# Performance work log

Hardware: AMD Instinct MI355X
Metric: run time of the kernel (lower is better)

The kernel has to match this reference:

```python
import jax, jax.numpy as jnp
import numpy as np

N, E, D, G = 100000, 600000, 128, 256  # nodes, edges, feat dim, num graphs
EPS = 1e-5


def graph_norm(x, batch, weight, bias, mean_scale):
    # PyG GraphNorm: per-graph mean/var with learnable mean_scale
    counts = jax.ops.segment_sum(jnp.ones((x.shape[0],), x.dtype), batch, num_segments=G)
    counts = jnp.maximum(counts, 1.0)[:, None]  # [G,1]
    mean = jax.ops.segment_sum(x, batch, num_segments=G) / counts  # [G,D]
    out = x - mean[batch] * mean_scale  # [N,D]
    var = jax.ops.segment_sum(out * out, batch, num_segments=G) / counts  # [G,D]
    inv_std = jax.lax.rsqrt(var + EPS)[batch]  # [N,D]
    return weight * out * inv_std + bias


def sage_conv_max(x, edge_index, w_l, b_l, w_r):
    # SAGEConv(aggr='max'): gather x[src], scatter-max into dst, then two linears
    src, dst = edge_index[0], edge_index[1]
    agg = jax.ops.segment_max(x[src], dst, num_segments=N)  # [N,D], -inf for empty
    agg = jnp.where(jnp.isfinite(agg), agg, 0.0)  # PyG fills empty segments with 0
    return agg @ w_l.T + b_l + x @ w_r.T


def setup_inputs() -> dict:
    key = jax.random.key(0)
    ks = jax.random.split(key, 6)
    x = jax.random.normal(ks[0], (N, D), dtype=jnp.float32)
    edge_index = jax.random.randint(ks[1], (2, E), 0, N, dtype=jnp.int64)
    batch = jnp.sort(jax.random.randint(ks[2], (N,), 0, G, dtype=jnp.int64))
    s = 1.0 / np.sqrt(D)
    return {
        "x": x,
        "edge_index": edge_index,
        "batch": batch,
        "n1_w": jnp.ones((D,), jnp.float32),
        "n1_b": jnp.zeros((D,), jnp.float32),
        "n1_ms": jnp.ones((D,), jnp.float32),
        "n2_w": jnp.ones((D,), jnp.float32),
        "n2_b": jnp.zeros((D,), jnp.float32),
        "n2_ms": jnp.ones((D,), jnp.float32),
        "w_l": jax.random.uniform(ks[3], (D, D), jnp.float32, -s, s),
        "b_l": jax.random.uniform(ks[4], (D,), jnp.float32, -s, s),
        "w_r": jax.random.uniform(ks[5], (D, D), jnp.float32, -s, s),
    }


def reference(x, edge_index, batch, n1_w, n1_b, n1_ms, n2_w, n2_b, n2_ms, w_l, b_l, w_r):
    h = graph_norm(x, batch, n1_w, n1_b, n1_ms)
    h = sage_conv_max(h, edge_index, w_l, b_l, w_r)
    h = jax.nn.relu(x + h)
    h = graph_norm(h, batch, n2_w, n2_b, n2_ms)
    return h
```

## Files before the change

### kernel.cpp

```cpp
#include <hip/hip_runtime.h>
#include <math.h>

#define NN 100000
#define EE 600000
#define DD 128
#define GG 256
#define EPSV 1e-5f

typedef __attribute__((ext_vector_type(8))) __bf16 bf16x8;
typedef __attribute__((ext_vector_type(16))) float f32x16;
typedef __attribute__((ext_vector_type(4))) unsigned short us4;

#define OFF_A1      0
#define OFF_B1      131072
#define OFF_A2      262144
#define OFF_B2      393216
#define OFF_DEG     524288
#define OFF_ROWPTR  924288
#define OFF_CURSOR  1324352
#define OFF_BSUMS   1724352
#define OFF_CNT     1726400
#define OFF_ELIST   1728448
#define OFF_WB      4128448
#define OFF_H1B     4193984
#define WS_NEED_A   (OFF_H1B + 25600000ULL)

#define NB_STATS 782
#define NB_EDGE  2344
#define NB_H1B   12500
#define NB1024   98
#define NT32     3125

__device__ __forceinline__ int lower_bound_i(const int* __restrict__ a, int n, int v) {
    int lo = 0, hi = n;
    while (lo < hi) { int mid = (lo + hi) >> 1; if (a[mid] < v) lo = mid + 1; else hi = mid; }
    return lo;
}

__device__ __forceinline__ unsigned short f2bf(float f) {
    unsigned int u = __float_as_uint(f);
    unsigned int r = u + 0x7fffu + ((u >> 16) & 1u);
    return (unsigned short)(r >> 16);
}

__device__ __forceinline__ void stats_body(
    const float* __restrict__ X, const int* __restrict__ batch,
    float* __restrict__ Sg, float* __restrict__ Qg, int blk)
{
    int t = threadIdx.x;
    int rl = t >> 5, fq = t & 31;
    int r0 = blk * 128;
    int rend = r0 + 128; if (rend > NN) rend = NN;
    __shared__ float ls[8 * 128];
    __shared__ float lq[8 * 128];
    int g0 = batch[r0], g1 = batch[rend - 1];
    const float4* X4 = (const float4*)X;
    for (int g = g0; g <= g1; ++g) {
        int sa = (g == g0) ? r0   : lower_bound_i(batch, NN, g);
        int sb = (g == g1) ? rend : lower_bound_i(batch, NN, g + 1);
        float s0 = 0.f, s1 = 0.f, s2 = 0.f, s3 = 0.f;
        float q0 = 0.f, q1 = 0.f, q2 = 0.f, q3 = 0.f;
        for (int r = sa + rl; r < sb; r += 8) {
            float4 v = X4[r * 32 + fq];
            s0 += v.x; s1 += v.y; s2 += v.z; s3 += v.w;
            q0 += v.x * v.x; q1 += v.y * v.y; q2 += v.z * v.z; q3 += v.w * v.w;
        }
        ls[rl * 128 + fq * 4 + 0] = s0; ls[rl * 128 + fq * 4 + 1] = s1;
        ls[rl * 128 + fq * 4 + 2] = s2; ls[rl * 128 + fq * 4 + 3] = s3;
        lq[rl * 128 + fq * 4 + 0] = q0; lq[rl * 128 + fq * 4 + 1] = q1;
        lq[rl * 128 + fq * 4 + 2] = q2; lq[rl * 128 + fq * 4 + 3] = q3;
        __syncthreads();
        if (t < 32) {
            #pragma unroll
            for (int k = 0; k < 4; k++) {
                float as = 0.f, aq = 0.f;
                #pragma unroll
                for (int j = 0; j < 8; j++) { as += ls[j * 128 + t * 4 + k]; aq += lq[j * 128 + t * 4 + k]; }
                atomicAdd(&Sg[g * DD + t * 4 + k], as);
                atomicAdd(&Qg[g * DD + t * 4 + k], aq);
            }
        }
        __syncthreads();
    }
}

__global__ __launch_bounds__(256) void stats_p1(
    const float* __restrict__ X, const int* __restrict__ batch,
    float* __restrict__ Sg, float* __restrict__ Qg)
{
    stats_body(X, batch, Sg, Qg, blockIdx.x);
}

__global__ __launch_bounds__(256) void statsdeg_kernel(
    const float* __restrict__ X, const int* __restrict__ batch,
    float* __restrict__ Sg, float* __restrict__ Qg,
    const int* __restrict__ dst, int* __restrict__ deg)
{
    int b = blockIdx.x;
    if (b < NB_STATS) { stats_body(X, batch, Sg, Qg, b); return; }
    int e = (b - NB_STATS) * 256 + threadIdx.x;
    if (e < EE) atomicAdd(&deg[dst[e]], 1);
}

__global__ __launch_bounds__(128) void finalize_kernel(
    const int* __restrict__ batch, float* S, float* Q,
    const float* __restrict__ w, const float* __restrict__ bb, const float* __restrict__ ms,
    unsigned short* __restrict__ wb, const float* __restrict__ wl, const float* __restrict__ wr,
    int* __restrict__ cnt, int doW)
{
    int g = blockIdx.x;
    if (g >= GG) {
        if (!doW) return;
        const float* W = (g == GG) ? wl : wr;
        int kofs = (g == GG) ? 0 : 128;
        for (int tt = threadIdx.x; tt < DD * 32; tt += 128) {
            int j = tt >> 5, k4 = tt & 31;
            float4 v = ((const float4*)W)[j * 32 + k4];
            us4 o = { f2bf(v.x), f2bf(v.y), f2bf(v.z), f2bf(v.w) };
            *(us4*)&wb[j * 256 + kofs + k4 * 4] = o;
        }
        return;
    }
    __shared__ int sh[2];
    if (threadIdx.x == 0) { sh[0] = lower_bound_i(batch, NN, g); sh[1] = lower_bound_i(batch, NN, g + 1); }
    __syncthreads();
    int c_n = sh[1] - sh[0];
    if (cnt && threadIdx.x == 0) cnt[g] = c_n;
    float c = (float)(c_n > 0 ? c_n : 1);
    float inv_c = 1.0f / c;
    int d = threadIdx.x;
    float m  = S[g * DD + d] * inv_c;
    float qm = Q[g * DD + d] * inv_c;
    float sc = ms[d];
    float var = qm - m * m * sc * (2.0f - sc);
    float Ad = w[d] * rsqrtf(var + EPSV);
    S[g * DD + d] = Ad;
    Q[g * DD + d] = bb[d] - Ad * m * sc;
}

__global__ __launch_bounds__(256) void h1bscan_kernel(
    const float* __restrict__ X, const int* __restrict__ batch,
    const float* __restrict__ A1, const float* __restrict__ B1, unsigned short* __restrict__ h1b,
    const int* __restrict__ deg, int* __restrict__ bsums)
{
    int blk = blockIdx.x;
    if (blk < NB_H1B) {
        int f = blk * 256 + threadIdx.x;
        int i = f >> 5, c = f & 31;
        int g = batch[i];
        float4 v = ((const float4*)X)[f];
        float4 a = ((const float4*)A1)[g * 32 + c];
        float4 b = ((const float4*)B1)[g * 32 + c];
        us4 o = { f2bf(fmaf(a.x, v.x, b.x)), f2bf(fmaf(a.y, v.y, b.y)),
                  f2bf(fmaf(a.z, v.z, b.z)), f2bf(fmaf(a.w, v.w, b.w)) };
        *(us4*)&h1b[i * DD + c * 4] = o;
        return;
    }
    int b = blk - NB_H1B, t = threadIdx.x;
    int base = b * 1024 + t * 4;
    int v = 0;
    #pragma unroll
    for (int k = 0; k < 4; k++) { int i = base + k; if (i < NN) v += deg[i]; }
    __shared__ int sd[256];
    sd[t] = v; __syncthreads();
    for (int off = 128; off > 0; off >>= 1) { if (t < off) sd[t] += sd[t + off]; __syncthreads(); }
    if (t == 0) bsums[b] = sd[0];
}

__global__ __launch_bounds__(256) void scan1(const int* __restrict__ deg, int* __restrict__ bsums) {
    int b = blockIdx.x, t = threadIdx.x;
    int base = b * 1024 + t * 4;
    int v = 0;
    #pragma unroll
    for (int k = 0; k < 4; k++) { int i = base + k; if (i < NN) v += deg[i]; }
    __shared__ int sd[256];
    sd[t] = v; __syncthreads();
    for (int off = 128; off > 0; off >>= 1) { if (t < off) sd[t] += sd[t + off]; __syncthreads(); }
    if (t == 0) bsums[b] = sd[0];
}

__global__ __launch_bounds__(256) void scan3(const int* __restrict__ deg, const int* __restrict__ bsums,
                                             int* __restrict__ rowptr, int* __restrict__ cursor) {
    int b = blockIdx.x, t = threadIdx.x;
    int boff = 0;
    for (int j = 0; j < b; j++) boff += bsums[j];
    int base = b * 1024 + t * 4;
    int d0 = 0, d1 = 0, d2 = 0, d3 = 0;
    if (base     < NN) d0 = deg[base];
    if (base + 1 < NN) d1 = deg[base + 1];
    if (base + 2 < NN) d2 = deg[base + 2];
    if (base + 3 < NN) d3 = deg[base + 3];
    int tsum = d0 + d1 + d2 + d3;
    __shared__ int sd[256];
    sd[t] = tsum; __syncthreads();
    for (int off = 1; off < 256; off <<= 1) {
        int a = (t >= off) ? sd[t - off] : 0;
        __syncthreads();
        sd[t] += a;
        __syncthreads();
    }
    int exc = sd[t] - tsum + boff;
    int p0 = exc, p1 = exc + d0, p2 = exc + d0 + d1, p3 = exc + d0 + d1 + d2;
    if (base     < NN) { rowptr[base]     = p0; cursor[base]     = p0; }
    if (base + 1 < NN) { rowptr[base + 1] = p1; cursor[base + 1] = p1; }
    if (base + 2 < NN) { rowptr[base + 2] = p2; cursor[base + 2] = p2; }
    if (base + 3 < NN) { rowptr[base + 3] = p3; cursor[base + 3] = p3; }
    if (b == 0 && t == 0) rowptr[NN] = EE;
}

__global__ __launch_bounds__(256) void fill_kernel(const int* __restrict__ src, const int* __restrict__ dst,
                                                   int* __restrict__ cursor, int* __restrict__ elist) {
    int e = blockIdx.x * 256 + threadIdx.x;
    if (e < EE) {
        int p = atomicAdd(&cursor[dst[e]], 1);
        elist[p] = src[e];
    }
}

#define USTR 264
__global__ __launch_bounds__(256) void gemm_mega(
    const float* __restrict__ X, const unsigned short* __restrict__ h1b,
    const int* __restrict__ batch, const int* __restrict__ rowptr, const int* __restrict__ elist,
    const unsigned short* __restrict__ wb, const float* __restrict__ blv,
    float* __restrict__ Sg2, float* __restrict__ Qg2, float* __restrict__ out)
{
    __shared__ unsigned short sU[32 * USTR];
    __shared__ int sBatch[32];
    int tid = threadIdx.x;
    int i0 = blockIdx.x * 32;
    int lane = tid & 63, wave = tid >> 6;
    int m = lane & 31, hf = lane >> 5;

    for (int t = tid; t < 32 * 16; t += 256) {
        int r = t >> 4, c = t & 15;
        int i = i0 + r; if (i >= NN) i = NN - 1;
        uint4 v = ((const uint4*)(h1b + (size_t)i * DD))[c];
        *(uint4*)&sU[r * USTR + 128 + c * 8] = v;
    }
    if (tid < 32) {
        int i = i0 + tid;
        sBatch[tid] = (i < NN) ? batch[i] : -1;
    }

    int hw = tid >> 5, j = tid & 31;
    for (int rr = hw; rr < 32; rr += 8) {
        int i = i0 + rr;
        int beg = 0, end = 0;
        if (i < NN) { beg = rowptr[i]; end = rowptr[i + 1]; }
        float a0 = -INFINITY, a1 = -INFINITY, a2 = -INFINITY, a3 = -INFINITY;
        int last = end - 1;
        for (int e = beg; e < end; e += 8) {
            int n[8];
            #pragma unroll
            for (int k = 0; k < 8; k++) { int t2 = e + k; n[k] = elist[t2 < last ? t2 : last]; }
            us4 p[8];
            #pragma unroll
            for (int k = 0; k < 8; k++) p[k] = *(const us4*)(h1b + (size_t)n[k] * DD + j * 4);
            #pragma unroll
            for (int k = 0; k < 8; k++) {
                a0 = fmaxf(a0, __uint_as_float((unsigned)p[k][0] << 16));
                a1 = fmaxf(a1, __uint_as_float((unsigned)p[k][1] << 16));
                a2 = fmaxf(a2, __uint_as_float((unsigned)p[k][2] << 16));
                a3 = fmaxf(a3, __uint_as_float((unsigned)p[k][3] << 16));
            }
        }
        us4 r4 = { 0, 0, 0, 0 };
        if (end > beg) {
            r4[0] = (unsigned short)(__float_as_uint(a0) >> 16);
            r4[1] = (unsigned short)(__float_as_uint(a1) >> 16);
            r4[2] = (unsigned short)(__float_as_uint(a2) >> 16);
            r4[3] = (unsigned short)(__float_as_uint(a3) >> 16);
        }
        *(us4*)&sU[rr * USTR + j * 4] = r4;
    }
    __syncthreads();

    int col = wave * 32 + m;
    const unsigned short* bcol = wb + col * 256 + hf * 8;
    const unsigned short* arow = &sU[m * USTR + hf * 8];

    f32x16 acc;
    #pragma unroll
    for (int r = 0; r < 16; r++) acc[r] = 0.f;
    #pragma unroll
    for (int s = 0; s < 16; s++) {
        bf16x8 b = *(const bf16x8*)(bcol + s * 16);
        bf16x8 a = *(const bf16x8*)(arow + s * 16);
        acc = __builtin_amdgcn_mfma_f32_32x32x16_bf16(a, b, acc, 0, 0, 0);
    }

    float blc = blv[col];
    float s_run = 0.f, q_run = 0.f;
    int cur_g = -1;
    #pragma unroll
    for (int reg = 0; reg < 16; reg++) {
        int rl = (reg & 3) + 8 * (reg >> 2) + 4 * hf;
        int i = i0 + rl;
        if (i < NN) {
            float v = X[i * DD + col] + blc + acc[reg];
            v = v > 0.f ? v : 0.f;
            out[i * DD + col] = v;
            int g = sBatch[rl];
            if (g != cur_g) {
                if (cur_g >= 0) {
                    atomicAdd(&Sg2[cur_g * DD + col], s_run);
                    atomicAdd(&Qg2[cur_g * DD + col], q_run);
                }
                cur_g = g; s_run = 0.f; q_run = 0.f;
            }
            s_run += v; q_run += v * v;
        }
    }
    if (cur_g >= 0) {
        atomicAdd(&Sg2[cur_g * DD + col], s_run);
        atomicAdd(&Qg2[cur_g * DD + col], q_run);
    }
}

__global__ __launch_bounds__(256) void apply_a(
    float* __restrict__ H, const int* __restrict__ batch,
    const float* __restrict__ Sg2, const float* __restrict__ Qg2, const int* __restrict__ cnt,
    const float* __restrict__ w2, const float* __restrict__ b2, const float* __restrict__ ms2)
{
    int f = blockIdx.x * 256 + threadIdx.x;
    if (f >= NN * 32) return;
    int i = f >> 5, c = f & 31;
    int g = batch[i];
    int cg = cnt[g];
    float invc = 1.0f / (float)(cg > 0 ? cg : 1);
    float4 S  = ((const float4*)Sg2)[g * 32 + c];
    float4 Q  = ((const float4*)Qg2)[g * 32 + c];
    float4 W  = ((const float4*)w2)[c];
    float4 Bv = ((const float4*)b2)[c];
    float4 Ms = ((const float4*)ms2)[c];
    float4 v = ((float4*)H)[f];
    {
        float mm = S.x * invc, qm = Q.x * invc;
        float A = W.x * rsqrtf(qm - mm * mm * Ms.x * (2.0f - Ms.x) + EPSV);
        v.x = fmaf(A, v.x, Bv.x - A * mm * Ms.x);
    }
    {
        float mm = S.y * invc, qm = Q.y * invc;
        float A = W.y * rsqrtf(qm - mm * mm * Ms.y * (2.0f - Ms.y) + EPSV);
        v.y = fmaf(A, v.y, Bv.y - A * mm * Ms.y);
    }
    {
        float mm = S.z * invc, qm = Q.z * invc;
        float A = W.z * rsqrtf(qm - mm * mm * Ms.z * (2.0f - Ms.z) + EPSV);
        v.z = fmaf(A, v.z, Bv.z - A * mm * Ms.z);
    }
    {
        float mm = S.w * invc, qm = Q.w * invc;
        float A = W.w * rsqrtf(qm - mm * mm * Ms.w * (2.0f - Ms.w) + EPSV);
        v.w = fmaf(A, v.w, Bv.w - A * mm * Ms.w);
    }
    ((float4*)H)[f] = v;
}

__global__ __launch_bounds__(256) void apply_b(float* __restrict__ H, const int* __restrict__ batch,
                                               const float* __restrict__ A2, const float* __restrict__ B2) {
    int f = blockIdx.x * 256 + threadIdx.x;
    if (f >= NN * 32) return;
    int i = f >> 5, c = f & 31;
    int g = batch[i];
    float4 v = ((float4*)H)[f];
    float4 a = ((const float4*)A2)[g * 32 + c];
    float4 b = ((const float4*)B2)[g * 32 + c];
    v.x = fmaf(a.x, v.x, b.x); v.y = fmaf(a.y, v.y, b.y);
    v.z = fmaf(a.z, v.z, b.z); v.w = fmaf(a.w, v.w, b.w);
    ((float4*)H)[f] = v;
}

__global__ __launch_bounds__(256) void agg_b(
    const float* __restrict__ X, const int* __restrict__ batch,
    const float* __restrict__ A1, const float* __restrict__ B1,
    const int* __restrict__ rowptr, const int* __restrict__ elist, float* __restrict__ H)
{
    int i = blockIdx.x * 2 + (threadIdx.x >> 7);
    int d = threadIdx.x & 127;
    int beg = rowptr[i], end = rowptr[i + 1];
    float acc = -INFINITY;
    int e = beg;
    for (; e + 2 <= end; e += 2) {
        int s0 = elist[e], s1 = elist[e + 1];
        int g0 = batch[s0], g1 = batch[s1];
        float v0 = fmaf(A1[g0 * DD + d], X[s0 * DD + d], B1[g0 * DD + d]);
        float v1 = fmaf(A1[g1 * DD + d], X[s1 * DD + d], B1[g1 * DD + d]);
        acc = fmaxf(acc, fmaxf(v0, v1));
    }
    for (; e < end; e++) {
        int s = elist[e]; int g = batch[s];
        acc = fmaxf(acc, fmaf(A1[g * DD + d], X[s * DD + d], B1[g * DD + d]));
    }
    if (end == beg) acc = 0.f;
    H[i * DD + d] = acc;
}

#define BM 128
#define LDT 72
__global__ __launch_bounds__(256) void gemm_b(
    const float* __restrict__ X, const int* __restrict__ batch,
    const float* __restrict__ A1, const float* __restrict__ B1,
    const float* __restrict__ wl, const float* __restrict__ blv, const float* __restrict__ wr,
    float* __restrict__ H)
{
    __shared__ unsigned short Ut[BM * LDT];
    __shared__ unsigned short Wt[DD * LDT];
    int i0 = blockIdx.x * BM;
    int tid = threadIdx.x;
    int lane = tid & 63, wave = tid >> 6;
    int wrow = (wave >> 1) * 64, wcol = (wave & 1) * 64;
    int m = lane & 31, hf = lane >> 5;

    f32x16 acc00, acc01, acc10, acc11;
    #pragma unroll
    for (int r = 0; r < 16; r++) { acc00[r] = 0.f; acc01[r] = 0.f; acc10[r] = 0.f; acc11[r] = 0.f; }

    for (int c = 0; c < 4; c++) {
        __syncthreads();
        for (int t = tid; t < BM * 16; t += 256) {
            int r = t >> 4, c4 = t & 15;
            int i = i0 + r; if (i >= NN) i = NN - 1;
            float4 v;
            if (c < 2) {
                v = ((const float4*)H)[i * 32 + c * 16 + c4];
            } else {
                int g = batch[i];
                float4 xv = ((const float4*)X)[i * 32 + (c - 2) * 16 + c4];
                float4 a = ((const float4*)A1)[g * 32 + (c - 2) * 16 + c4];
                float4 b = ((const float4*)B1)[g * 32 + (c - 2) * 16 + c4];
                v.x = fmaf(a.x, xv.x, b.x); v.y = fmaf(a.y, xv.y, b.y);
                v.z = fmaf(a.z, xv.z, b.z); v.w = fmaf(a.w, xv.w, b.w);
            }
            us4 o = { f2bf(v.x), f2bf(v.y), f2bf(v.z), f2bf(v.w) };
            *(us4*)&Ut[r * LDT + c4 * 4] = o;
        }
        {
            const float* Wsrc = (c < 2) ? wl : wr;
            int kb = (c & 1) * 16;
            for (int t = tid; t < DD * 16; t += 256) {
                int j = t >> 4, c4 = t & 15;
                float4 v = ((const float4*)Wsrc)[j * 32 + kb + c4];
                us4 o = { f2bf(v.x), f2bf(v.y), f2bf(v.z), f2bf(v.w) };
                *(us4*)&Wt[j * LDT + c4 * 4] = o;
            }
        }
        __syncthreads();
        #pragma unroll
        for (int kk = 0; kk < 4; kk++) {
            int kb2 = kk * 16 + hf * 8;
            bf16x8 a0 = *(const bf16x8*)&Ut[(wrow      + m) * LDT + kb2];
            bf16x8 a1 = *(const bf16x8*)&Ut[(wrow + 32 + m) * LDT + kb2];
            bf16x8 b0 = *(const bf16x8*)&Wt[(wcol      + m) * LDT + kb2];
            bf16x8 b1 = *(const bf16x8*)&Wt[(wcol + 32 + m) * LDT + kb2];
            acc00 = __builtin_amdgcn_mfma_f32_32x32x16_bf16(a0, b0, acc00, 0, 0, 0);
            acc01 = __builtin_amdgcn_mfma_f32_32x32x16_bf16(a0, b1, acc01, 0, 0, 0);
            acc10 = __builtin_amdgcn_mfma_f32_32x32x16_bf16(a1, b0, acc10, 0, 0, 0);
            acc11 = __builtin_amdgcn_mfma_f32_32x32x16_bf16(a1, b1, acc11, 0, 0, 0);
        }
    }

    int col0 = wcol + m, col1 = wcol + 32 + m;
    float bl0 = blv[col0], bl1 = blv[col1];
    #pragma unroll
    for (int reg = 0; reg < 16; reg++) {
        int rl = (reg & 3) + 8 * (reg >> 2) + 4 * hf;
        int ia = i0 + wrow + rl;
        int ib = i0 + wrow + 32 + rl;
        if (ia < NN) {
            float v0 = X[ia * DD + col0] + bl0 + acc00[reg];
            float v1 = X[ia * DD + col1] + bl1 + acc01[reg];
            H[ia * DD + col0] = v0 > 0.f ? v0 : 0.f;
            H[ia * DD + col1] = v1 > 0.f ? v1 : 0.f;
        }
        if (ib < NN) {
            float v0 = X[ib * DD + col0] + bl0 + acc10[reg];
            float v1 = X[ib * DD + col1] + bl1 + acc11[reg];
            H[ib * DD + col0] = v0 > 0.f ? v0 : 0.f;
            H[ib * DD + col1] = v1 > 0.f ? v1 : 0.f;
        }
    }
}

extern "C" void kernel_launch(void* const* d_in, const int* in_sizes, int n_in,
                              void* d_out, int out_size, void* d_ws, size_t ws_size,
                              hipStream_t stream) {
    const float* x    = (const float*)d_in[0];
    const int*   ei   = (const int*)d_in[1];
    const int*   batch= (const int*)d_in[2];
    const float* n1w  = (const float*)d_in[3];
    const float* n1b  = (const float*)d_in[4];
    const float* n1ms = (const float*)d_in[5];
    const float* n2w  = (const float*)d_in[6];
    const float* n2b  = (const float*)d_in[7];
    const float* n2ms = (const float*)d_in[8];
    const float* wl   = (const float*)d_in[9];
    const float* bl   = (const float*)d_in[10];
    const float* wr   = (const float*)d_in[11];
    float* out = (float*)d_out;

    char* w = (char*)d_ws;
    float* A1     = (float*)(w + OFF_A1);
    float* B1     = (float*)(w + OFF_B1);
    float* A2     = (float*)(w + OFF_A2);
    float* B2     = (float*)(w + OFF_B2);
    int*   deg    = (int*)(w + OFF_DEG);
    int*   rowptr = (int*)(w + OFF_ROWPTR);
    int*   cursor = (int*)(w + OFF_CURSOR);
    int*   bsums  = (int*)(w + OFF_BSUMS);
    int*   cnt    = (int*)(w + OFF_CNT);
    int*   elist  = (int*)(w + OFF_ELIST);
    unsigned short* wb  = (unsigned short*)(w + OFF_WB);
    unsigned short* h1b = (unsigned short*)(w + OFF_H1B);

    const int* src = ei;
    const int* dst = ei + EE;
    bool bigws = (ws_size >= WS_NEED_A);

    hipMemsetAsync(w, 0, OFF_ROWPTR, stream);

    statsdeg_kernel<<<NB_STATS + NB_EDGE, 256, 0, stream>>>(x, batch, A1, B1, dst, deg);
    finalize_kernel<<<GG + 2, 128, 0, stream>>>(batch, A1, B1, n1w, n1b, n1ms,
                                                wb, wl, wr, cnt, bigws ? 1 : 0);

    if (bigws) {
        h1bscan_kernel<<<NB_H1B + NB1024, 256, 0, stream>>>(x, batch, A1, B1, h1b, deg, bsums);
        scan3<<<NB1024, 256, 0, stream>>>(deg, bsums, rowptr, cursor);
        fill_kernel<<<NB_EDGE, 256, 0, stream>>>(src, dst, cursor, elist);

        gemm_mega<<<NT32, 256, 0, stream>>>(x, h1b, batch, rowptr, elist,
                                            wb, bl, A2, B2, out);

        apply_a<<<NB_H1B, 256, 0, stream>>>(out, batch, A2, B2, cnt, n2w, n2b, n2ms);
    } else {
        scan1<<<NB1024, 256, 0, stream>>>(deg, bsums);
        scan3<<<NB1024, 256, 0, stream>>>(deg, bsums, rowptr, cursor);
        fill_kernel<<<NB_EDGE, 256, 0, stream>>>(src, dst, cursor, elist);

        agg_b<<<NN / 2, 256, 0, stream>>>(x, batch, A1, B1, rowptr, elist, out);
        gemm_b<<<(NN + BM - 1) / BM, 256, 0, stream>>>(x, batch, A1, B1, wl, bl, wr, out);

        stats_p1<<<NB_STATS, 256, 0, stream>>>(out, batch, A2, B2);
        finalize_kernel<<<GG, 128, 0, stream>>>(batch, A2, B2, n2w, n2b, n2ms,
                                                (unsigned short*)nullptr,
                                                (const float*)nullptr, (const float*)nullptr,
                                                (int*)nullptr, 0);
        apply_b<<<NB_H1B, 256, 0, stream>>>(out, batch, A2, B2);
    }
}
```

Measured before the change: 300.4 us.

## Split neighbor max-aggregation out of fused GEMM into its own kernel

```diff
diff --git a/kernel.cpp b/kernel.cpp
--- a/kernel.cpp
+++ b/kernel.cpp
@@ -30,6 +30,7 @@
 #define NB_H1B   12500
 #define NB1024   98
 #define NT32     3125
+#define NB_AGG   12500
 
 __device__ __forceinline__ int lower_bound_i(const int* __restrict__ a, int n, int v) {
     int lo = 0, hi = n;
@@ -217,10 +218,46 @@
     }
 }
 
+__global__ __launch_bounds__(256) void aggmax_kernel(
+    const unsigned short* __restrict__ h1b,
+    const int* __restrict__ rowptr, const int* __restrict__ elist,
+    unsigned short* __restrict__ aggb)
+{
+    int hw = threadIdx.x >> 5;
+    int j  = threadIdx.x & 31;
+    int i  = blockIdx.x * 8 + hw;
+    int beg = rowptr[i], end = rowptr[i + 1];
+    float a0 = -INFINITY, a1 = -INFINITY, a2 = -INFINITY, a3 = -INFINITY;
+    int last = end - 1;
+    for (int e = beg; e < end; e += 8) {
+        int n[8];
+        #pragma unroll
+        for (int k = 0; k < 8; k++) { int t2 = e + k; n[k] = elist[t2 < last ? t2 : last]; }
+        us4 p[8];
+        #pragma unroll
+        for (int k = 0; k < 8; k++) p[k] = *(const us4*)(h1b + (size_t)n[k] * DD + j * 4);
+        #pragma unroll
+        for (int k = 0; k < 8; k++) {
+            a0 = fmaxf(a0, __uint_as_float((unsigned)p[k][0] << 16));
+            a1 = fmaxf(a1, __uint_as_float((unsigned)p[k][1] << 16));
+            a2 = fmaxf(a2, __uint_as_float((unsigned)p[k][2] << 16));
+            a3 = fmaxf(a3, __uint_as_float((unsigned)p[k][3] << 16));
+        }
+    }
+    us4 r4 = { 0, 0, 0, 0 };
+    if (end > beg) {
+        r4[0] = (unsigned short)(__float_as_uint(a0) >> 16);
+        r4[1] = (unsigned short)(__float_as_uint(a1) >> 16);
+        r4[2] = (unsigned short)(__float_as_uint(a2) >> 16);
+        r4[3] = (unsigned short)(__float_as_uint(a3) >> 16);
+    }
+    *(us4*)&aggb[(size_t)i * 256 + j * 4] = r4;
+}
+
 #define USTR 264
 __global__ __launch_bounds__(256) void gemm_mega(
     const float* __restrict__ X, const unsigned short* __restrict__ h1b,
-    const int* __restrict__ batch, const int* __restrict__ rowptr, const int* __restrict__ elist,
+    const int* __restrict__ batch,
     const unsigned short* __restrict__ wb, const float* __restrict__ blv,
     float* __restrict__ Sg2, float* __restrict__ Qg2, float* __restrict__ out)
 {
@@ -230,49 +267,21 @@
     int i0 = blockIdx.x * 32;
     int lane = tid & 63, wave = tid >> 6;
     int m = lane & 31, hf = lane >> 5;
-
-    for (int t = tid; t < 32 * 16; t += 256) {
-        int r = t >> 4, c = t & 15;
-        int i = i0 + r; if (i >= NN) i = NN - 1;
-        uint4 v = ((const uint4*)(h1b + (size_t)i * DD))[c];
-        *(uint4*)&sU[r * USTR + 128 + c * 8] = v;
-    }
-    if (tid < 32) {
-        int i = i0 + tid;
-        sBatch[tid] = (i < NN) ? batch[i] : -1;
-    }
-
-    int hw = tid >> 5, j = tid & 31;
-    for (int rr = hw; rr < 32; rr += 8) {
-        int i = i0 + rr;
-        int beg = 0, end = 0;
-        if (i < NN) { beg = rowptr[i]; end = rowptr[i + 1]; }
-        float a0 = -INFINITY, a1 = -INFINITY, a2 = -INFINITY, a3 = -INFINITY;
-        int last = end - 1;
-        for (int e = beg; e < end; e += 8) {
-            int n[8];
-            #pragma unroll
-            for (int k = 0; k < 8; k++) { int t2 = e + k; n[k] = elist[t2 < last ? t2 : last]; }
-            us4 p[8];
-            #pragma unroll
-            for (int k = 0; k < 8; k++) p[k] = *(const us4*)(h1b + (size_t)n[k] * DD + j * 4);
-            #pragma unroll
-            for (int k = 0; k < 8; k++) {
-                a0 = fmaxf(a0, __uint_as_float((unsigned)p[k][0] << 16));
-                a1 = fmaxf(a1, __uint_as_float((unsigned)p[k][1] << 16));
-                a2 = fmaxf(a2, __uint_as_float((unsigned)p[k][2] << 16));
-                a3 = fmaxf(a3, __uint_as_float((unsigned)p[k][3] << 16));
-            }
-        }
-        us4 r4 = { 0, 0, 0, 0 };
-        if (end > beg) {
-            r4[0] = (unsigned short)(__float_as_uint(a0) >> 16);
-            r4[1] = (unsigned short)(__float_as_uint(a1) >> 16);
-            r4[2] = (unsigned short)(__float_as_uint(a2) >> 16);
-            r4[3] = (unsigned short)(__float_as_uint(a3) >> 16);
-        }
-        *(us4*)&sU[rr * USTR + j * 4] = r4;
-    }
+    const unsigned short* aggb = (const unsigned short*)out;
+
+    for (int t = tid; t < 32 * 32; t += 256) {
+        int r = t >> 5, c = t & 31;
+        int i = i0 + r;
+        uint4 v;
+        if (c < 16) {
+            v = ((const uint4*)(aggb + (size_t)i * 256))[c];
+            *(uint4*)&sU[r * USTR + c * 8] = v;
+        } else {
+            v = ((const uint4*)(h1b + (size_t)i * DD))[c - 16];
+            *(uint4*)&sU[r * USTR + 128 + (c - 16) * 8] = v;
+        }
+    }
+    if (tid < 32) sBatch[tid] = batch[i0 + tid];
     __syncthreads();
 
     int col = wave * 32 + m;
@@ -296,20 +305,18 @@
     for (int reg = 0; reg < 16; reg++) {
         int rl = (reg & 3) + 8 * (reg >> 2) + 4 * hf;
         int i = i0 + rl;
-        if (i < NN) {
-            float v = X[i * DD + col] + blc + acc[reg];
-            v = v > 0.f ? v : 0.f;
-            out[i * DD + col] = v;
-            int g = sBatch[rl];
-            if (g != cur_g) {
-                if (cur_g >= 0) {
-                    atomicAdd(&Sg2[cur_g * DD + col], s_run);
-                    atomicAdd(&Qg2[cur_g * DD + col], q_run);
-                }
-                cur_g = g; s_run = 0.f; q_run = 0.f;
+        float v = X[i * DD + col] + blc + acc[reg];
+        v = v > 0.f ? v : 0.f;
+        out[i * DD + col] = v;
+        int g = sBatch[rl];
+        if (g != cur_g) {
+            if (cur_g >= 0) {
+                atomicAdd(&Sg2[cur_g * DD + col], s_run);
+                atomicAdd(&Qg2[cur_g * DD + col], q_run);
             }
-            s_run += v; q_run += v * v;
-        }
+            cur_g = g; s_run = 0.f; q_run = 0.f;
+        }
+        s_run += v; q_run += v * v;
     }
     if (cur_g >= 0) {
         atomicAdd(&Sg2[cur_g * DD + col], s_run);
@@ -528,8 +535,9 @@
         scan3<<<NB1024, 256, 0, stream>>>(deg, bsums, rowptr, cursor);
         fill_kernel<<<NB_EDGE, 256, 0, stream>>>(src, dst, cursor, elist);
 
-        gemm_mega<<<NT32, 256, 0, stream>>>(x, h1b, batch, rowptr, elist,
-                                            wb, bl, A2, B2, out);
+        aggmax_kernel<<<NB_AGG, 256, 0, stream>>>(h1b, rowptr, elist, (unsigned short*)out);
+
+        gemm_mega<<<NT32, 256, 0, stream>>>(x, h1b, batch, wb, bl, A2, B2, out);
 
         apply_a<<<NB_H1B, 256, 0, stream>>>(out, batch, A2, B2, cnt, n2w, n2b, n2ms);
     } else {
```

After: 304.4 us. About the same (+1.3%).
